# Performance work log

Measured on AMD Instinct MI355X. Metric: run time of the kernel, lower is better.

## Reference

```python
import jax, jax.numpy as jnp
import numpy as np

B, N, F, NCG, NCONV, VOCAB = 16, 1024, 128, 64, 3, 100
EPS = 0.001


def setup_inputs() -> dict:
    key = jax.random.key(0)
    ks = jax.random.split(key, 16)
    atoms_nodes = jax.random.randint(ks[0], (B, N), 0, VOCAB, dtype=jnp.int32)
    xyz = jax.random.normal(ks[1], (B, N, 3), jnp.float32) * 3.0
    # chain bonds (i, i+1) per molecule -> every atom has degree >= 1
    bi = jnp.repeat(jnp.arange(B), N - 1)
    si = jnp.tile(jnp.arange(N - 1), B)
    bonds = jnp.stack([bi, si, si + 1], axis=1).astype(jnp.int32)  # [B*(N-1), 3]
    tau = jnp.float32(1.0)
    gumbel_u = jax.random.uniform(ks[2], (B, N, NCG), jnp.float32, 1e-6, 1.0 - 1e-6)
    # parameters
    emb = jax.random.normal(ks[3], (VOCAB, F), jnp.float32) * 0.1
    emb = emb.at[0].set(0.0)  # padding_idx=0
    s = 1.0 / np.sqrt(F)
    upd_W1 = jax.random.uniform(ks[4], (NCONV, F, F), jnp.float32, -s, s)
    upd_b1 = jax.random.uniform(ks[5], (NCONV, F), jnp.float32, -s, s)
    upd_W2 = jax.random.uniform(ks[6], (NCONV, F, F), jnp.float32, -s, s)
    upd_b2 = jax.random.uniform(ks[7], (NCONV, F), jnp.float32, -s, s)
    cg_W1 = jax.random.uniform(ks[8], (F, F), jnp.float32, -s, s)
    cg_b1 = jax.random.uniform(ks[9], (F,), jnp.float32, -s, s)
    cg_W2 = jax.random.uniform(ks[10], (F, NCG), jnp.float32, -s, s)
    cg_b2 = jax.random.uniform(ks[11], (NCG,), jnp.float32, -s, s)
    return {"atoms_nodes": atoms_nodes, "xyz": xyz, "bonds": bonds, "tau": tau,
            "gumbel_u": gumbel_u, "emb": emb,
            "upd_W1": upd_W1, "upd_b1": upd_b1, "upd_W2": upd_W2, "upd_b2": upd_b2,
            "cg_W1": cg_W1, "cg_b1": cg_b1, "cg_W2": cg_W2, "cg_b2": cg_b2}


def reference(atoms_nodes, xyz, bonds, tau, gumbel_u, emb,
              upd_W1, upd_b1, upd_W2, upd_b2, cg_W1, cg_b1, cg_W2, cg_b2):
    h = emb[atoms_nodes]  # [B,N,F]
    # dense symmetric adjacency from bond list
    adj = jnp.zeros((B, N, N), jnp.float32)
    adj = adj.at[bonds[:, 0], bonds[:, 1], bonds[:, 2]].set(1.0)
    adj = adj.at[bonds[:, 0], bonds[:, 2], bonds[:, 1]].set(1.0)
    deg = jnp.sum(adj, axis=-1)[:, :, None]  # [B,N,1]
    for l in range(NCONV):
        ch = jnp.tanh(h @ upd_W1[l] + upd_b1[l]) @ upd_W2[l] + upd_b2[l]
        dh = jnp.einsum('bif,bij->bjf', ch, adj) / deg
        h = h + dh
    # gumbel-softmax assignment (soft)
    assign_logits = jnp.tanh(h @ cg_W1 + cg_b1) @ cg_W2 + cg_b2  # [B,N,NCG]
    g = -jnp.log(-jnp.log(gumbel_u))
    M = jax.nn.softmax((assign_logits + g) / tau, axis=-1)  # [B,N,NCG]
    M_norm = M / jnp.sum(M, axis=-2, keepdims=True)
    H = jnp.einsum('bnj,bnf->bjf', M_norm, h)        # [B,NCG,F]
    cg_xyz = jnp.einsum('bin,bij->bjn', xyz, M_norm)  # [B,NCG,3]
    cg_adj = jnp.broadcast_to(jnp.ones((NCG, NCG)) - jnp.eye(NCG), (B, NCG, NCG))
    diff = cg_xyz[:, :, None, :] - cg_xyz[:, None, :, :]
    dist = jnp.sqrt(jnp.sum(diff * diff, axis=-1) + EPS)  # [B,NCG,NCG]
    knbrs = jnp.argsort(dist, axis=-1)
    return (M, M_norm, h, H, adj, cg_xyz, cg_adj, knbrs)
```

## Files before the change

### kernel.cpp

```cpp
#include <hip/hip_runtime.h>
#include <math.h>

#define BB 16
#define NN 1024
#define FF 128
#define NCG 64
#define NCONV 3
#define CAP 8

typedef double f64x4 __attribute__((ext_vector_type(4)));

static const size_t O_M     = 0;
static const size_t O_MN    = (size_t)BB*NN*NCG;
static const size_t O_H     = O_MN  + (size_t)BB*NN*NCG;
static const size_t O_HH    = O_H   + (size_t)BB*NN*FF;
static const size_t O_ADJ   = O_HH  + (size_t)BB*NCG*FF;
static const size_t O_CGXYZ = O_ADJ + (size_t)BB*NN*NN;
static const size_t O_CGADJ = O_CGXYZ + (size_t)BB*NCG*3;
static const size_t O_KN    = O_CGADJ + (size_t)BB*NCG*NCG;

static const size_t S_H64   = 0;
static const size_t S_T64   = 2097152;
static const size_t S_C64   = 4194304;
static const size_t S_LM64  = 0;
static const size_t S_COLSP = 4194304;
static const size_t S_HPF   = 6291456;
static const size_t S_CGP   = 7340032;
static const size_t S_NBR   = 7438336;
static const size_t S_W64   = 7503872;

static const size_t WO_CGW1 = 98304;
static const size_t WO_CGW2 = 114688;
static const int    W64_N   = 122880;

static const size_t W_INVD = 0;
static const size_t W_COLS = (size_t)BB*NN;
static const size_t W_CG64 = W_COLS + (size_t)BB*NCG;
static const size_t W_CNT  = W_CG64 + (size_t)BB*NCG*3;

__global__ void k_zero(int* cnt) {
    int i = blockIdx.x * blockDim.x + threadIdx.x;
    if (i < BB*NN) cnt[i] = 0;
}

__global__ void k_build_nbr(const int* __restrict__ bonds, int nb, int* cnt, int* nbr) {
    int i = blockIdx.x * blockDim.x + threadIdx.x;
    if (i >= nb) return;
    int b = bonds[i*3+0], s = bonds[i*3+1], t = bonds[i*3+2];
    int ns = b*NN + s, nt = b*NN + t;
    int p = atomicAdd(&cnt[ns], 1);
    if (p < CAP) nbr[(size_t)ns*CAP + p] = nt;
    int q = atomicAdd(&cnt[nt], 1);
    if (q < CAP) nbr[(size_t)nt*CAP + q] = ns;
}

__global__ void k_invdeg(const int* __restrict__ cnt, double* invdeg) {
    int i = blockIdx.x * blockDim.x + threadIdx.x;
    if (i >= BB*NN) return;
    int d = cnt[i];
    invdeg[i] = d > 0 ? 1.0 / (double)d : 0.0;
}

__global__ void k_cgadj(float* cgadj) {
    int idx = blockIdx.x * blockDim.x + threadIdx.x;
    if (idx >= BB*NCG*NCG) return;
    int i = (idx / NCG) % NCG, j = idx % NCG;
    cgadj[idx] = (i == j) ? 0.f : 1.f;
}

__global__ void k_emb64(const int* __restrict__ atoms, const float* __restrict__ emb,
                        double* __restrict__ h) {
    int idx = blockIdx.x * blockDim.x + threadIdx.x;
    if (idx >= BB*NN*(FF/4)) return;
    int n = idx / (FF/4), f4 = idx % (FF/4);
    int a = atoms[n];
    const float4 v = *reinterpret_cast<const float4*>(&emb[(size_t)a*FF + f4*4]);
    double* hp = &h[(size_t)n*FF + f4*4];
    hp[0] = (double)v.x; hp[1] = (double)v.y; hp[2] = (double)v.z; hp[3] = (double)v.w;
}

__global__ void k_cvtW(const float* __restrict__ uW1, const float* __restrict__ uW2,
                       const float* __restrict__ cgW1, const float* __restrict__ cgW2,
                       double* __restrict__ W64) {
    int idx = blockIdx.x * blockDim.x + threadIdx.x;
    if (idx >= W64_N) return;
    float v;
    if (idx < 98304) {
        int l = idx >> 15, r = idx & 32767;
        v = (r < 16384) ? uW1[l*16384 + r] : uW2[l*16384 + (r & 16383)];
    } else if (idx < 114688) {
        v = cgW1[idx - 98304];
    } else {
        v = cgW2[idx - 114688];
    }
    W64[idx] = (double)v;
}

template<int COUTT, bool TANH>
__global__ __launch_bounds__(256) void k_gemm_mfma(const double* __restrict__ in,
                                                   const double* __restrict__ W,
                                                   const float* __restrict__ bias,
                                                   double* __restrict__ out) {
    constexpr int K = 128, KC = 32;
    constexpr int CT2 = COUTT/2;
    __shared__ double As[64*34];
    __shared__ double Ws[KC*66];
    const int tid = threadIdx.x;
    const int col0 = blockIdx.y * 64;
    const int C02 = col0 >> 1;
    const size_t row0 = (size_t)blockIdx.x * 64;
    const double2* in2 = reinterpret_cast<const double2*>(in + row0*K);
    const double2* Wg2 = reinterpret_cast<const double2*>(W);
    double2* As2 = reinterpret_cast<double2*>(As);
    double2* Ws2 = reinterpret_cast<double2*>(Ws);

    double2 pA[4], pW[4];
    #pragma unroll
    for (int i = 0; i < 4; ++i) { int q = tid + i*256; pA[i] = in2[(q>>4)*64 + (q&15)]; }
    #pragma unroll
    for (int i = 0; i < 4; ++i) { int q = tid + i*256; pW[i] = Wg2[(q>>5)*CT2 + C02 + (q&31)]; }

    const int lane = tid & 63;
    const int wv = tid >> 6;
    const int m = lane & 15, kq = lane >> 4;
    const int arow = (wv*16 + m)*34 + kq;

    f64x4 acc[4];
    #pragma unroll
    for (int ct = 0; ct < 4; ++ct) acc[ct] = (f64x4){0.0, 0.0, 0.0, 0.0};

    for (int kc = 0; kc < K; kc += KC) {
        __syncthreads();
        #pragma unroll
        for (int i = 0; i < 4; ++i) { int q = tid + i*256; As2[(q>>4)*17 + (q&15)] = pA[i]; }
        #pragma unroll
        for (int i = 0; i < 4; ++i) { int q = tid + i*256; Ws2[(q>>5)*33 + (q&31)] = pW[i]; }
        if (kc + KC < K) {
            const int kn = kc + KC, kn2 = kn >> 1;
            #pragma unroll
            for (int i = 0; i < 4; ++i) { int q = tid + i*256; pA[i] = in2[(q>>4)*64 + kn2 + (q&15)]; }
            #pragma unroll
            for (int i = 0; i < 4; ++i) { int q = tid + i*256; pW[i] = Wg2[(kn + (q>>5))*CT2 + C02 + (q&31)]; }
        }
        __syncthreads();
        #pragma unroll
        for (int kk = 0; kk < KC; kk += 4) {
            double a = As[arow + kk];
            const double* wrow = Ws + (kk + kq)*66 + m;
            #pragma unroll
            for (int ct = 0; ct < 4; ++ct) {
                double b = wrow[ct*16];
                acc[ct] = __builtin_amdgcn_mfma_f64_16x16x4f64(a, b, acc[ct], 0, 0, 0);
            }
        }
    }

    const int orow = wv*16 + kq*4;
    #pragma unroll
    for (int ct = 0; ct < 4; ++ct) {
        int c = col0 + ct*16 + m;
        double bv = (double)bias[c];
        #pragma unroll
        for (int i = 0; i < 4; ++i) {
            double v = acc[ct][i] + bv;
            if (TANH) v = tanh(v);
            out[(row0 + orow + i)*COUTT + c] = v;
        }
    }
}

template<bool WRITE_F32>
__global__ void k_gather(const double* __restrict__ ch, const double* __restrict__ invdeg,
                         const int* __restrict__ nbr, const int* __restrict__ cnt,
                         double* __restrict__ h, float* __restrict__ hout) {
    int idx = blockIdx.x * blockDim.x + threadIdx.x;
    if (idx >= BB*NN*(FF/4)) return;
    int node = idx >> 5, f4 = idx & 31;
    int c = cnt[node];
    double2 s0; s0.x = 0.0; s0.y = 0.0;
    double2 s1 = s0;
    for (int q = 0; q < c; ++q) {
        int nb = nbr[(size_t)node*CAP + q];
        const double2* cp = reinterpret_cast<const double2*>(ch + (size_t)nb*FF + f4*4);
        double2 a = cp[0], b2 = cp[1];
        s0.x += a.x; s0.y += a.y; s1.x += b2.x; s1.y += b2.y;
    }
    double w = invdeg[node];
    double2* hp = reinterpret_cast<double2*>(h + (size_t)node*FF + f4*4);
    double2 h0 = hp[0], h1 = hp[1];
    h0.x += s0.x*w; h0.y += s0.y*w; h1.x += s1.x*w; h1.y += s1.y*w;
    hp[0] = h0; hp[1] = h1;
    if (WRITE_F32) {
        float4 o; o.x = (float)h0.x; o.y = (float)h0.y; o.z = (float)h1.x; o.w = (float)h1.y;
        *reinterpret_cast<float4*>(&hout[(size_t)node*FF + f4*4]) = o;
    }
}

__global__ void k_softmax64(double* __restrict__ lm, const float* __restrict__ gum,
                            const float* __restrict__ tau_p, float* __restrict__ M_out) {
    int row = blockIdx.x * 4 + threadIdx.x / 64;
    int lane = threadIdx.x & 63;
    double tau = (double)(*tau_p);
    double u = (double)gum[(size_t)row*NCG + lane];
    double g = -log(-log(u));
    double v = (lm[(size_t)row*NCG + lane] + g) / tau;
    double m = v;
    #pragma unroll
    for (int off = 32; off; off >>= 1) m = fmax(m, __shfl_xor(m, off));
    double e = exp(v - m);
    double s = e;
    #pragma unroll
    for (int off = 32; off; off >>= 1) s += __shfl_xor(s, off);
    double mv = e / s;
    lm[(size_t)row*NCG + lane] = mv;
    M_out[(size_t)row*NCG + lane] = (float)mv;
}

__global__ __launch_bounds__(256) void k_cols_part(const double* __restrict__ M,
                                                   double* __restrict__ colsp) {
    __shared__ double red[256];
    const int b = blockIdx.x, c = blockIdx.y;
    const int tid = threadIdx.x;
    const int j = tid & 63, q = tid >> 6;
    const double* Mb = M + (size_t)b*NN*NCG + (size_t)(c*64 + q*16)*NCG;
    double s = 0.0;
    #pragma unroll
    for (int r = 0; r < 16; ++r) s += Mb[(size_t)r*NCG + j];
    red[tid] = s;
    __syncthreads();
    if (tid < 64)
        colsp[((size_t)b*16 + c)*NCG + j] = red[j] + red[64+j] + red[128+j] + red[192+j];
}

__global__ void k_cols_fin(const double* __restrict__ colsp, double* __restrict__ colsum) {
    int idx = blockIdx.x * blockDim.x + threadIdx.x;
    if (idx >= BB*NCG) return;
    int b = idx >> 6, j = idx & 63;
    double s = 0.0;
    #pragma unroll
    for (int c = 0; c < 16; ++c) s += colsp[((size_t)b*16 + c)*NCG + j];
    colsum[idx] = s;
}

__global__ void k_mnorm_out(const double* __restrict__ M, const double* __restrict__ colsum,
                            float* __restrict__ Mn) {
    size_t i = (size_t)blockIdx.x * blockDim.x + threadIdx.x;
    if (i >= (size_t)BB*NN*NCG) return;
    size_t b = i >> 16;
    int j = (int)(i & 63);
    Mn[i] = (float)(M[i] / colsum[b*NCG + j]);
}

__global__ __launch_bounds__(256) void k_Hpart32(const float* __restrict__ Mn,
                                                 const float* __restrict__ h,
                                                 float* __restrict__ Hp) {
    __shared__ float Ms[32*NCG];
    __shared__ float hs[32*FF];
    const int b = blockIdx.x, ch = blockIdx.y;
    const int tid = threadIdx.x;
    const int tc = tid % 32, tr = tid / 32;
    const float4* M4 = reinterpret_cast<const float4*>(Mn + (size_t)b*NN*NCG);
    const float4* h4 = reinterpret_cast<const float4*>(h + (size_t)b*NN*FF);
    float4* Ms4 = reinterpret_cast<float4*>(Ms);
    float4* hs4 = reinterpret_cast<float4*>(hs);
    const float2* Ms2 = reinterpret_cast<const float2*>(Ms);
    const float2* hs2 = reinterpret_cast<const float2*>(hs);

    float acc[8][4];
    #pragma unroll
    for (int i = 0; i < 8; ++i)
        #pragma unroll
        for (int j = 0; j < 4; ++j) acc[i][j] = 0.f;

    for (int s = 0; s < 2; ++s) {
        const int n0 = ch*64 + s*32;
        __syncthreads();
        #pragma unroll
        for (int i = 0; i < 2; ++i) Ms4[tid + i*256] = M4[n0*16 + tid + i*256];
        #pragma unroll
        for (int i = 0; i < 4; ++i) hs4[tid + i*256] = h4[n0*32 + tid + i*256];
        __syncthreads();
        for (int n = 0; n < 32; ++n) {
            float2 hv0 = hs2[n*64 + tc];
            float2 hv1 = hs2[n*64 + 32 + tc];
            float2 m0 = Ms2[n*32 + tr];
            float2 m1 = Ms2[n*32 + 8 + tr];
            float2 m2 = Ms2[n*32 + 16 + tr];
            float2 m3 = Ms2[n*32 + 24 + tr];
            float mj[8] = {m0.x, m0.y, m1.x, m1.y, m2.x, m2.y, m3.x, m3.y};
            #pragma unroll
            for (int jj = 0; jj < 8; ++jj) {
                acc[jj][0] += mj[jj]*hv0.x; acc[jj][1] += mj[jj]*hv0.y;
                acc[jj][2] += mj[jj]*hv1.x; acc[jj][3] += mj[jj]*hv1.y;
            }
        }
    }
    float* Ho = Hp + ((size_t)ch*BB + b) * NCG * FF;
    #pragma unroll
    for (int gj = 0; gj < 4; ++gj)
        #pragma unroll
        for (int pj = 0; pj < 2; ++pj) {
            int j = tr*2 + gj*16 + pj;
            int jj = gj*2 + pj;
            float2 o0; o0.x = acc[jj][0]; o0.y = acc[jj][1];
            float2 o1; o1.x = acc[jj][2]; o1.y = acc[jj][3];
            float2* op = reinterpret_cast<float2*>(Ho + (size_t)j*FF);
            op[tc] = o0; op[32 + tc] = o1;
        }
}

__global__ void k_Hfin32(const float* __restrict__ Hp, float* __restrict__ H) {
    int idx = blockIdx.x * blockDim.x + threadIdx.x;
    if (idx >= BB*NCG*FF) return;
    int b = idx / (NCG*FF);
    int r = idx % (NCG*FF);
    float s = 0.f;
    #pragma unroll
    for (int c = 0; c < 16; ++c) s += Hp[((size_t)c*BB + b)*NCG*FF + r];
    H[idx] = s;
}

__global__ __launch_bounds__(192) void k_cgpart(const double* __restrict__ M,
                                                const float* __restrict__ xyz,
                                                double* __restrict__ cgp) {
    __shared__ double Ms[32*NCG];
    __shared__ double xs[32*3];
    const int b = blockIdx.x, ch = blockIdx.y;
    const int tid = threadIdx.x;
    const int j = tid / 3, d = tid % 3;
    const int n0 = ch*32;
    const double2* M2 = reinterpret_cast<const double2*>(M + (size_t)b*NN*NCG);
    double2* Ms2 = reinterpret_cast<double2*>(Ms);
    const float* xb = xyz + (size_t)b*NN*3;
    for (int q = tid; q < 1024; q += 192) Ms2[q] = M2[n0*32 + q];
    for (int q = tid; q < 96; q += 192) xs[q] = (double)xb[n0*3 + q];
    __syncthreads();
    double acc = 0.0;
    #pragma unroll 8
    for (int n = 0; n < 32; ++n) acc += Ms[n*NCG + j] * xs[n*3 + d];
    cgp[((size_t)ch*BB + b)*192 + tid] = acc;
}

__global__ void k_cgfin(const double* __restrict__ cgp, const double* __restrict__ colsum,
                        double* __restrict__ cg64, float* __restrict__ cg) {
    int idx = blockIdx.x * blockDim.x + threadIdx.x;
    if (idx >= BB*NCG*3) return;
    int b = idx / (NCG*3);
    int r = idx % (NCG*3);
    int j = r / 3;
    double s = 0.0;
    #pragma unroll
    for (int c = 0; c < 32; ++c) s += cgp[((size_t)c*BB + b)*192 + r];
    double v = s / colsum[b*NCG + j];
    cg64[idx] = v;
    cg[idx] = (float)v;
}

__global__ __launch_bounds__(1024) void k_knbrs(const double* __restrict__ cg,
                                                float* __restrict__ kn) {
    __shared__ double cs[NCG*3];
    const int b = blockIdx.x;
    const int tid = threadIdx.x;
    const int i = blockIdx.y * 16 + tid / 64;
    const int j = tid & 63;
    if (tid < NCG*3) cs[tid] = cg[(size_t)b*NCG*3 + tid];
    __syncthreads();
    double xi = cs[i*3+0], yi = cs[i*3+1], zi = cs[i*3+2];
    double dxj = xi - cs[j*3+0], dyj = yi - cs[j*3+1], dzj = zi - cs[j*3+2];
    double d2j = dxj*dxj + dyj*dyj + dzj*dzj;
    int rank = 0;
    for (int k = 0; k < NCG; ++k) {
        double dx = xi - cs[k*3+0], dy = yi - cs[k*3+1], dz = zi - cs[k*3+2];
        double d2k = dx*dx + dy*dy + dz*dz;
        rank += (d2k < d2j) || (d2k == d2j && k < j);
    }
    kn[(size_t)b*NCG*NCG + (size_t)i*NCG + rank] = (float)j;
}

__global__ void k_zero_adj(float4* adj4, long n4) {
    long i = (long)blockIdx.x * blockDim.x + threadIdx.x;
    long stride = (long)gridDim.x * blockDim.x;
    float4 z; z.x = z.y = z.z = z.w = 0.f;
    for (; i < n4; i += stride) adj4[i] = z;
}

__global__ void k_bonds_adj(const int* __restrict__ bonds, int nb, float* adj) {
    int i = blockIdx.x * blockDim.x + threadIdx.x;
    if (i >= nb) return;
    int b = bonds[i*3+0], s = bonds[i*3+1], t = bonds[i*3+2];
    size_t base = (size_t)b * NN * NN;
    adj[base + (size_t)s*NN + t] = 1.f;
    adj[base + (size_t)t*NN + s] = 1.f;
}

extern "C" void kernel_launch(void* const* d_in, const int* in_sizes, int n_in,
                              void* d_out, int out_size, void* d_ws, size_t ws_size,
                              hipStream_t stream) {
    const int*   atoms  = (const int*)  d_in[0];
    const float* xyz    = (const float*)d_in[1];
    const int*   bonds  = (const int*)  d_in[2];
    const float* tau    = (const float*)d_in[3];
    const float* gum    = (const float*)d_in[4];
    const float* emb    = (const float*)d_in[5];
    const float* uW1    = (const float*)d_in[6];
    const float* ub1    = (const float*)d_in[7];
    const float* uW2    = (const float*)d_in[8];
    const float* ub2    = (const float*)d_in[9];
    const float* cgW1   = (const float*)d_in[10];
    const float* cgb1   = (const float*)d_in[11];
    const float* cgW2   = (const float*)d_in[12];
    const float* cgb2   = (const float*)d_in[13];

    float* out = (float*)d_out;
    float* o_M   = out + O_M;
    float* o_Mn  = out + O_MN;
    float* o_h   = out + O_H;
    float* o_H   = out + O_HH;
    float* o_adj = out + O_ADJ;
    float* o_cg  = out + O_CGXYZ;
    float* o_ca  = out + O_CGADJ;
    float* o_kn  = out + O_KN;

    double* scr   = (double*)o_adj;
    double* h64   = scr + S_H64;
    double* t64   = scr + S_T64;
    double* c64   = scr + S_C64;
    double* lm64  = scr + S_LM64;
    double* colsp = scr + S_COLSP;
    float*  Hpf   = (float*)(scr + S_HPF);
    double* cgp   = scr + S_CGP;
    int*    nbr   = (int*)(scr + S_NBR);
    double* W64   = scr + S_W64;

    double* wsd    = (double*)d_ws;
    double* invdeg = wsd + W_INVD;
    double* colsum = wsd + W_COLS;
    double* cg64   = wsd + W_CG64;
    int*    cnt    = (int*)(wsd + W_CNT);

    const int nb = in_sizes[2] / 3;

    hipLaunchKernelGGL(k_zero, dim3(64), dim3(256), 0, stream, cnt);
    hipLaunchKernelGGL(k_build_nbr, dim3((nb+255)/256), dim3(256), 0, stream,
                       bonds, nb, cnt, nbr);
    hipLaunchKernelGGL(k_invdeg, dim3(64), dim3(256), 0, stream, cnt, invdeg);
    hipLaunchKernelGGL(k_cgadj, dim3(256), dim3(256), 0, stream, o_ca);
    hipLaunchKernelGGL(k_cvtW, dim3((W64_N+255)/256), dim3(256), 0, stream,
                       uW1, uW2, cgW1, cgW2, W64);
    hipLaunchKernelGGL(k_emb64, dim3(2048), dim3(256), 0, stream, atoms, emb, h64);

    for (int l = 0; l < NCONV; ++l) {
        hipLaunchKernelGGL((k_gemm_mfma<128,true>), dim3(256,2), dim3(256), 0, stream,
                           h64, W64 + (size_t)l*32768, ub1 + (size_t)l*FF, t64);
        hipLaunchKernelGGL((k_gemm_mfma<128,false>), dim3(256,2), dim3(256), 0, stream,
                           t64, W64 + (size_t)l*32768 + 16384, ub2 + (size_t)l*FF, c64);
        if (l < NCONV-1)
            hipLaunchKernelGGL((k_gather<false>), dim3(2048), dim3(256), 0, stream,
                               c64, invdeg, nbr, cnt, h64, o_h);
        else
            hipLaunchKernelGGL((k_gather<true>), dim3(2048), dim3(256), 0, stream,
                               c64, invdeg, nbr, cnt, h64, o_h);
    }

    hipLaunchKernelGGL((k_gemm_mfma<128,true>), dim3(256,2), dim3(256), 0, stream,
                       h64, W64 + WO_CGW1, cgb1, t64);
    hipLaunchKernelGGL((k_gemm_mfma<64,false>), dim3(256,1), dim3(256), 0, stream,
                       t64, W64 + WO_CGW2, cgb2, lm64);

    hipLaunchKernelGGL(k_softmax64, dim3(4096), dim3(256), 0, stream,
                       lm64, gum, tau, o_M);
    hipLaunchKernelGGL(k_cols_part, dim3(16,16), dim3(256), 0, stream, lm64, colsp);
    hipLaunchKernelGGL(k_cols_fin, dim3(4), dim3(256), 0, stream, colsp, colsum);
    hipLaunchKernelGGL(k_mnorm_out, dim3(4096), dim3(256), 0, stream, lm64, colsum, o_Mn);
    hipLaunchKernelGGL(k_Hpart32, dim3(BB, 16), dim3(256), 0, stream, o_Mn, o_h, Hpf);
    hipLaunchKernelGGL(k_Hfin32, dim3(512), dim3(256), 0, stream, Hpf, o_H);
    hipLaunchKernelGGL(k_cgpart, dim3(BB, 32), dim3(192), 0, stream, lm64, xyz, cgp);
    hipLaunchKernelGGL(k_cgfin, dim3(12), dim3(256), 0, stream, cgp, colsum, cg64, o_cg);
    hipLaunchKernelGGL(k_knbrs, dim3(BB, 4), dim3(1024), 0, stream, cg64, o_kn);

    hipLaunchKernelGGL(k_zero_adj, dim3(4096), dim3(256), 0, stream,
                       (float4*)o_adj, (long)BB*NN*NN/4);
    hipLaunchKernelGGL(k_bonds_adj, dim3((nb+255)/256), dim3(256), 0, stream,
                       bonds, nb, o_adj);
}
```

Baseline: 369.8 us.

## Fuse neighbor gather into next GEMM, merge init kernels, atomic column sums

Folds the neighbor aggregation and h update of each conv layer into the A-tile load of the following tanh GEMM. That GEMM is either the next layer's first linear or the cg_W1 projection. This removes a separate gather pass and one re-read of h. The small setup kernels (zeroing, weight conversion, cg_adj fill, embedding) are merged into one launch, and invdeg is computed inline. Column sums of M are accumulated with double atomics inside the softmax kernel instead of a two-stage reduction. The trade-offs are a smaller 32-row GEMM tile, irregular gathers inside the GEMM prologue, and atomic contention on 1024 addresses.

```diff
diff --git a/kernel.cpp b/kernel.cpp
--- a/kernel.cpp
+++ b/kernel.cpp
@@ -23,7 +23,6 @@
 static const size_t S_T64   = 2097152;
 static const size_t S_C64   = 4194304;
 static const size_t S_LM64  = 0;
-static const size_t S_COLSP = 4194304;
 static const size_t S_HPF   = 6291456;
 static const size_t S_CGP   = 7340032;
 static const size_t S_NBR   = 7438336;
@@ -33,14 +32,39 @@
 static const size_t WO_CGW2 = 114688;
 static const int    W64_N   = 122880;
 
-static const size_t W_INVD = 0;
-static const size_t W_COLS = (size_t)BB*NN;
-static const size_t W_CG64 = W_COLS + (size_t)BB*NCG;
+static const size_t W_COLS = 0;
+static const size_t W_CG64 = (size_t)BB*NCG;
 static const size_t W_CNT  = W_CG64 + (size_t)BB*NCG*3;
 
-__global__ void k_zero(int* cnt) {
+__global__ void k_init(const int* __restrict__ atoms, const float* __restrict__ emb,
+                       const float* __restrict__ uW1, const float* __restrict__ uW2,
+                       const float* __restrict__ cgW1, const float* __restrict__ cgW2,
+                       double* __restrict__ W64, float* __restrict__ cgadj,
+                       int* __restrict__ cnt, double* __restrict__ colsum,
+                       double* __restrict__ h64) {
     int i = blockIdx.x * blockDim.x + threadIdx.x;
     if (i < BB*NN) cnt[i] = 0;
+    if (i < BB*NCG) colsum[i] = 0.0;
+    if (i < W64_N) {
+        float v;
+        if (i < 98304) {
+            int l = i >> 15, r = i & 32767;
+            v = (r < 16384) ? uW1[l*16384 + r] : uW2[l*16384 + (r & 16383)];
+        } else if (i < 114688) v = cgW1[i - 98304];
+        else                   v = cgW2[i - 114688];
+        W64[i] = (double)v;
+    }
+    if (i < BB*NCG*NCG) {
+        int r = (i / NCG) % NCG, cjj = i % NCG;
+        cgadj[i] = (r == cjj) ? 0.f : 1.f;
+    }
+    if (i < BB*NN*(FF/4)) {
+        int n = i / (FF/4), f4 = i % (FF/4);
+        int a = atoms[n];
+        const float4 v = *reinterpret_cast<const float4*>(&emb[(size_t)a*FF + f4*4]);
+        double* hp = &h64[(size_t)n*FF + f4*4];
+        hp[0] = (double)v.x; hp[1] = (double)v.y; hp[2] = (double)v.z; hp[3] = (double)v.w;
+    }
 }
 
 __global__ void k_build_nbr(const int* __restrict__ bonds, int nb, int* cnt, int* nbr) {
@@ -52,48 +76,6 @@
     if (p < CAP) nbr[(size_t)ns*CAP + p] = nt;
     int q = atomicAdd(&cnt[nt], 1);
     if (q < CAP) nbr[(size_t)nt*CAP + q] = ns;
-}
-
-__global__ void k_invdeg(const int* __restrict__ cnt, double* invdeg) {
-    int i = blockIdx.x * blockDim.x + threadIdx.x;
-    if (i >= BB*NN) return;
-    int d = cnt[i];
-    invdeg[i] = d > 0 ? 1.0 / (double)d : 0.0;
-}
-
-__global__ void k_cgadj(float* cgadj) {
-    int idx = blockIdx.x * blockDim.x + threadIdx.x;
-    if (idx >= BB*NCG*NCG) return;
-    int i = (idx / NCG) % NCG, j = idx % NCG;
-    cgadj[idx] = (i == j) ? 0.f : 1.f;
-}
-
-__global__ void k_emb64(const int* __restrict__ atoms, const float* __restrict__ emb,
-                        double* __restrict__ h) {
-    int idx = blockIdx.x * blockDim.x + threadIdx.x;
-    if (idx >= BB*NN*(FF/4)) return;
-    int n = idx / (FF/4), f4 = idx % (FF/4);
-    int a = atoms[n];
-    const float4 v = *reinterpret_cast<const float4*>(&emb[(size_t)a*FF + f4*4]);
-    double* hp = &h[(size_t)n*FF + f4*4];
-    hp[0] = (double)v.x; hp[1] = (double)v.y; hp[2] = (double)v.z; hp[3] = (double)v.w;
-}
-
-__global__ void k_cvtW(const float* __restrict__ uW1, const float* __restrict__ uW2,
-                       const float* __restrict__ cgW1, const float* __restrict__ cgW2,
-                       double* __restrict__ W64) {
-    int idx = blockIdx.x * blockDim.x + threadIdx.x;
-    if (idx >= W64_N) return;
-    float v;
-    if (idx < 98304) {
-        int l = idx >> 15, r = idx & 32767;
-        v = (r < 16384) ? uW1[l*16384 + r] : uW2[l*16384 + (r & 16383)];
-    } else if (idx < 114688) {
-        v = cgW1[idx - 98304];
-    } else {
-        v = cgW2[idx - 114688];
-    }
-    W64[idx] = (double)v;
 }
 
 template<int COUTT, bool TANH>
@@ -169,35 +151,108 @@
     }
 }
 
-template<bool WRITE_F32>
-__global__ void k_gather(const double* __restrict__ ch, const double* __restrict__ invdeg,
-                         const int* __restrict__ nbr, const int* __restrict__ cnt,
-                         double* __restrict__ h, float* __restrict__ hout) {
-    int idx = blockIdx.x * blockDim.x + threadIdx.x;
-    if (idx >= BB*NN*(FF/4)) return;
-    int node = idx >> 5, f4 = idx & 31;
-    int c = cnt[node];
-    double2 s0; s0.x = 0.0; s0.y = 0.0;
-    double2 s1 = s0;
-    for (int q = 0; q < c; ++q) {
-        int nb = nbr[(size_t)node*CAP + q];
-        const double2* cp = reinterpret_cast<const double2*>(ch + (size_t)nb*FF + f4*4);
-        double2 a = cp[0], b2 = cp[1];
-        s0.x += a.x; s0.y += a.y; s1.x += b2.x; s1.y += b2.y;
-    }
-    double w = invdeg[node];
-    double2* hp = reinterpret_cast<double2*>(h + (size_t)node*FF + f4*4);
-    double2 h0 = hp[0], h1 = hp[1];
-    h0.x += s0.x*w; h0.y += s0.y*w; h1.x += s1.x*w; h1.y += s1.y*w;
-    hp[0] = h0; hp[1] = h1;
-    if (WRITE_F32) {
-        float4 o; o.x = (float)h0.x; o.y = (float)h0.y; o.z = (float)h1.x; o.w = (float)h1.y;
-        *reinterpret_cast<float4*>(&hout[(size_t)node*FF + f4*4]) = o;
+template<bool GATHER, bool WRITE_F32>
+__global__ __launch_bounds__(256) void k_gemm_fg(const double* __restrict__ in,
+        const double* __restrict__ ch, const int* __restrict__ nbr,
+        const int* __restrict__ cnt, const double* __restrict__ W,
+        const float* __restrict__ bias, double* __restrict__ hupd,
+        float* __restrict__ hf32, double* __restrict__ out) {
+    constexpr int K = 128, KC = 32, AST = 130, WST = 130;
+    __shared__ double As[32*AST];
+    __shared__ double Ws[KC*WST];
+    const int tid = threadIdx.x;
+    const size_t row0 = (size_t)blockIdx.x * 32;
+    const double2* Wg2 = reinterpret_cast<const double2*>(W);
+
+    double2 pW[8];
+    #pragma unroll
+    for (int i = 0; i < 8; ++i) { int q = tid + i*256; pW[i] = Wg2[q]; }
+
+    {
+        const int srow = tid >> 3, skg = tid & 7;
+        const size_t grow = row0 + srow;
+        double2 v[8];
+        const double2* hp = reinterpret_cast<const double2*>(in + grow*K) + skg*8;
+        #pragma unroll
+        for (int i = 0; i < 8; ++i) v[i] = hp[i];
+        if (GATHER) {
+            int c = cnt[grow];
+            double w = c > 0 ? 1.0/(double)c : 0.0;
+            for (int q = 0; q < c; ++q) {
+                int nb2 = nbr[grow*CAP + q];
+                const double2* cp = reinterpret_cast<const double2*>(ch + (size_t)nb2*K) + skg*8;
+                #pragma unroll
+                for (int i = 0; i < 8; ++i) { double2 t = cp[i]; v[i].x += w*t.x; v[i].y += w*t.y; }
+            }
+            double2* hg = reinterpret_cast<double2*>(hupd + grow*K) + skg*8;
+            #pragma unroll
+            for (int i = 0; i < 8; ++i) hg[i] = v[i];
+        }
+        if (WRITE_F32) {
+            float4* fp = reinterpret_cast<float4*>(hf32 + grow*K) + skg*4;
+            #pragma unroll
+            for (int i = 0; i < 4; ++i) {
+                float4 o;
+                o.x = (float)v[2*i].x;   o.y = (float)v[2*i].y;
+                o.z = (float)v[2*i+1].x; o.w = (float)v[2*i+1].y;
+                fp[i] = o;
+            }
+        }
+        double2* ap = reinterpret_cast<double2*>(As + srow*AST) + skg*8;
+        #pragma unroll
+        for (int i = 0; i < 8; ++i) ap[i] = v[i];
+    }
+
+    const int lane = tid & 63, wv = tid >> 6;
+    const int wr = wv & 1, wc = wv >> 1;
+    const int m = lane & 15, kq = lane >> 4;
+    const int abase = (wr*16 + m)*AST;
+
+    f64x4 acc[4];
+    #pragma unroll
+    for (int ct = 0; ct < 4; ++ct) acc[ct] = (f64x4){0.0, 0.0, 0.0, 0.0};
+
+    for (int kc = 0; kc < K; kc += KC) {
+        __syncthreads();
+        #pragma unroll
+        for (int i = 0; i < 8; ++i) {
+            int q = tid + i*256;
+            reinterpret_cast<double2*>(Ws + (q>>6)*WST)[q & 63] = pW[i];
+        }
+        if (kc + KC < K) {
+            #pragma unroll
+            for (int i = 0; i < 8; ++i) {
+                int q = tid + i*256;
+                pW[i] = Wg2[(kc + KC + (q>>6))*64 + (q & 63)];
+            }
+        }
+        __syncthreads();
+        #pragma unroll
+        for (int kk = 0; kk < KC; kk += 4) {
+            double a = As[abase + kc + kk + kq];
+            const double* wrow = Ws + (kk + kq)*WST + wc*64 + m;
+            #pragma unroll
+            for (int ct = 0; ct < 4; ++ct) {
+                double b = wrow[ct*16];
+                acc[ct] = __builtin_amdgcn_mfma_f64_16x16x4f64(a, b, acc[ct], 0, 0, 0);
+            }
+        }
+    }
+
+    const int orow = wr*16 + kq*4;
+    #pragma unroll
+    for (int ct = 0; ct < 4; ++ct) {
+        int c = wc*64 + ct*16 + m;
+        double bv = (double)bias[c];
+        #pragma unroll
+        for (int i = 0; i < 4; ++i)
+            out[(row0 + orow + i)*K + c] = tanh(acc[ct][i] + bv);
     }
 }
 
 __global__ void k_softmax64(double* __restrict__ lm, const float* __restrict__ gum,
-                            const float* __restrict__ tau_p, float* __restrict__ M_out) {
+                            const float* __restrict__ tau_p, float* __restrict__ M_out,
+                            double* __restrict__ colsum) {
     int row = blockIdx.x * 4 + threadIdx.x / 64;
     int lane = threadIdx.x & 63;
     double tau = (double)(*tau_p);
@@ -214,32 +269,7 @@
     double mv = e / s;
     lm[(size_t)row*NCG + lane] = mv;
     M_out[(size_t)row*NCG + lane] = (float)mv;
-}
-
-__global__ __launch_bounds__(256) void k_cols_part(const double* __restrict__ M,
-                                                   double* __restrict__ colsp) {
-    __shared__ double red[256];
-    const int b = blockIdx.x, c = blockIdx.y;
-    const int tid = threadIdx.x;
-    const int j = tid & 63, q = tid >> 6;
-    const double* Mb = M + (size_t)b*NN*NCG + (size_t)(c*64 + q*16)*NCG;
-    double s = 0.0;
-    #pragma unroll
-    for (int r = 0; r < 16; ++r) s += Mb[(size_t)r*NCG + j];
-    red[tid] = s;
-    __syncthreads();
-    if (tid < 64)
-        colsp[((size_t)b*16 + c)*NCG + j] = red[j] + red[64+j] + red[128+j] + red[192+j];
-}
-
-__global__ void k_cols_fin(const double* __restrict__ colsp, double* __restrict__ colsum) {
-    int idx = blockIdx.x * blockDim.x + threadIdx.x;
-    if (idx >= BB*NCG) return;
-    int b = idx >> 6, j = idx & 63;
-    double s = 0.0;
-    #pragma unroll
-    for (int c = 0; c < 16; ++c) s += colsp[((size_t)b*16 + c)*NCG + j];
-    colsum[idx] = s;
+    atomicAdd(&colsum[(row >> 10) * NCG + lane], mv);
 }
 
 __global__ void k_mnorm_out(const double* __restrict__ M, const double* __restrict__ colsum,
@@ -426,51 +456,42 @@
     double* t64   = scr + S_T64;
     double* c64   = scr + S_C64;
     double* lm64  = scr + S_LM64;
-    double* colsp = scr + S_COLSP;
     float*  Hpf   = (float*)(scr + S_HPF);
     double* cgp   = scr + S_CGP;
     int*    nbr   = (int*)(scr + S_NBR);
     double* W64   = scr + S_W64;
 
     double* wsd    = (double*)d_ws;
-    double* invdeg = wsd + W_INVD;
     double* colsum = wsd + W_COLS;
     double* cg64   = wsd + W_CG64;
     int*    cnt    = (int*)(wsd + W_CNT);
 
     const int nb = in_sizes[2] / 3;
 
-    hipLaunchKernelGGL(k_zero, dim3(64), dim3(256), 0, stream, cnt);
+    hipLaunchKernelGGL(k_init, dim3(2048), dim3(256), 0, stream,
+                       atoms, emb, uW1, uW2, cgW1, cgW2, W64, o_ca, cnt, colsum, h64);
     hipLaunchKernelGGL(k_build_nbr, dim3((nb+255)/256), dim3(256), 0, stream,
                        bonds, nb, cnt, nbr);
-    hipLaunchKernelGGL(k_invdeg, dim3(64), dim3(256), 0, stream, cnt, invdeg);
-    hipLaunchKernelGGL(k_cgadj, dim3(256), dim3(256), 0, stream, o_ca);
-    hipLaunchKernelGGL(k_cvtW, dim3((W64_N+255)/256), dim3(256), 0, stream,
-                       uW1, uW2, cgW1, cgW2, W64);
-    hipLaunchKernelGGL(k_emb64, dim3(2048), dim3(256), 0, stream, atoms, emb, h64);
-
-    for (int l = 0; l < NCONV; ++l) {
-        hipLaunchKernelGGL((k_gemm_mfma<128,true>), dim3(256,2), dim3(256), 0, stream,
-                           h64, W64 + (size_t)l*32768, ub1 + (size_t)l*FF, t64);
-        hipLaunchKernelGGL((k_gemm_mfma<128,false>), dim3(256,2), dim3(256), 0, stream,
-                           t64, W64 + (size_t)l*32768 + 16384, ub2 + (size_t)l*FF, c64);
-        if (l < NCONV-1)
-            hipLaunchKernelGGL((k_gather<false>), dim3(2048), dim3(256), 0, stream,
-                               c64, invdeg, nbr, cnt, h64, o_h);
-        else
-            hipLaunchKernelGGL((k_gather<true>), dim3(2048), dim3(256), 0, stream,
-                               c64, invdeg, nbr, cnt, h64, o_h);
-    }
 
     hipLaunchKernelGGL((k_gemm_mfma<128,true>), dim3(256,2), dim3(256), 0, stream,
-                       h64, W64 + WO_CGW1, cgb1, t64);
+                       h64, W64, ub1, t64);
+    hipLaunchKernelGGL((k_gemm_mfma<128,false>), dim3(256,2), dim3(256), 0, stream,
+                       t64, W64 + 16384, ub2, c64);
+    hipLaunchKernelGGL((k_gemm_fg<true,false>), dim3(512), dim3(256), 0, stream,
+                       h64, c64, nbr, cnt, W64 + 32768, ub1 + FF, h64, o_h, t64);
+    hipLaunchKernelGGL((k_gemm_mfma<128,false>), dim3(256,2), dim3(256), 0, stream,
+                       t64, W64 + 32768 + 16384, ub2 + FF, c64);
+    hipLaunchKernelGGL((k_gemm_fg<true,false>), dim3(512), dim3(256), 0, stream,
+                       h64, c64, nbr, cnt, W64 + 65536, ub1 + 2*FF, h64, o_h, t64);
+    hipLaunchKernelGGL((k_gemm_mfma<128,false>), dim3(256,2), dim3(256), 0, stream,
+                       t64, W64 + 65536 + 16384, ub2 + 2*FF, c64);
+    hipLaunchKernelGGL((k_gemm_fg<true,true>), dim3(512), dim3(256), 0, stream,
+                       h64, c64, nbr, cnt, W64 + WO_CGW1, cgb1, h64, o_h, t64);
     hipLaunchKernelGGL((k_gemm_mfma<64,false>), dim3(256,1), dim3(256), 0, stream,
                        t64, W64 + WO_CGW2, cgb2, lm64);
 
     hipLaunchKernelGGL(k_softmax64, dim3(4096), dim3(256), 0, stream,
-                       lm64, gum, tau, o_M);
-    hipLaunchKernelGGL(k_cols_part, dim3(16,16), dim3(256), 0, stream, lm64, colsp);
-    hipLaunchKernelGGL(k_cols_fin, dim3(4), dim3(256), 0, stream, colsp, colsum);
+                       lm64, gum, tau, o_M, colsum);
     hipLaunchKernelGGL(k_mnorm_out, dim3(4096), dim3(256), 0, stream, lm64, colsum, o_Mn);
     hipLaunchKernelGGL(k_Hpart32, dim3(BB, 16), dim3(256), 0, stream, o_Mn, o_h, Hpf);
     hipLaunchKernelGGL(k_Hfin32, dim3(512), dim3(256), 0, stream, Hpf, o_H);
```

After: 380.8 us. 1.03x slower.

## Fuse init kernels, fold column sums into softmax, build adjacency from neighbor lists

Applied to the files above, without the earlier changes.

Merges the zero, weight conversion, cg_adj fill and embedding kernels into one init launch. The inverse degree is now computed inside the gather, and column sums are accumulated with atomics inside the softmax kernel. The cg_xyz finalize is folded into the knbrs kernel. The separate zero-fill plus bond scatter of the dense adjacency becomes one per-row kernel that writes zeros and ones from the neighbor list. This cuts launch count and one full pass over the 64 MB adjacency, at the cost of nondeterministic atomic summation order and a CAP-limited neighbor list defining the adjacency.

```diff
diff --git a/kernel.cpp b/kernel.cpp
--- a/kernel.cpp
+++ b/kernel.cpp
@@ -23,24 +23,47 @@
 static const size_t S_T64   = 2097152;
 static const size_t S_C64   = 4194304;
 static const size_t S_LM64  = 0;
-static const size_t S_COLSP = 4194304;
 static const size_t S_HPF   = 6291456;
 static const size_t S_CGP   = 7340032;
-static const size_t S_NBR   = 7438336;
 static const size_t S_W64   = 7503872;
 
 static const size_t WO_CGW1 = 98304;
 static const size_t WO_CGW2 = 114688;
 static const int    W64_N   = 122880;
 
-static const size_t W_INVD = 0;
-static const size_t W_COLS = (size_t)BB*NN;
-static const size_t W_CG64 = W_COLS + (size_t)BB*NCG;
-static const size_t W_CNT  = W_CG64 + (size_t)BB*NCG*3;
-
-__global__ void k_zero(int* cnt) {
+static const size_t W_COLS = 0;
+static const size_t W_CNT  = (size_t)BB*NCG;
+static const size_t W_NBR  = W_CNT + (size_t)BB*NN/2;
+
+__global__ void k_init(const int* __restrict__ atoms, const float* __restrict__ emb,
+                       const float* __restrict__ uW1, const float* __restrict__ uW2,
+                       const float* __restrict__ cgW1, const float* __restrict__ cgW2,
+                       double* __restrict__ W64, float* __restrict__ cgadj,
+                       int* __restrict__ cnt, double* __restrict__ colsum,
+                       double* __restrict__ h64) {
     int i = blockIdx.x * blockDim.x + threadIdx.x;
     if (i < BB*NN) cnt[i] = 0;
+    if (i < BB*NCG) colsum[i] = 0.0;
+    if (i < W64_N) {
+        float v;
+        if (i < 98304) {
+            int l = i >> 15, r = i & 32767;
+            v = (r < 16384) ? uW1[l*16384 + r] : uW2[l*16384 + (r & 16383)];
+        } else if (i < 114688) v = cgW1[i - 98304];
+        else                   v = cgW2[i - 114688];
+        W64[i] = (double)v;
+    }
+    if (i < BB*NCG*NCG) {
+        int r = (i / NCG) % NCG, cjj = i % NCG;
+        cgadj[i] = (r == cjj) ? 0.f : 1.f;
+    }
+    if (i < BB*NN*(FF/4)) {
+        int n = i / (FF/4), f4 = i % (FF/4);
+        int a = atoms[n];
+        const float4 v = *reinterpret_cast<const float4*>(&emb[(size_t)a*FF + f4*4]);
+        double* hp = &h64[(size_t)n*FF + f4*4];
+        hp[0] = (double)v.x; hp[1] = (double)v.y; hp[2] = (double)v.z; hp[3] = (double)v.w;
+    }
 }
 
 __global__ void k_build_nbr(const int* __restrict__ bonds, int nb, int* cnt, int* nbr) {
@@ -52,48 +75,6 @@
     if (p < CAP) nbr[(size_t)ns*CAP + p] = nt;
     int q = atomicAdd(&cnt[nt], 1);
     if (q < CAP) nbr[(size_t)nt*CAP + q] = ns;
-}
-
-__global__ void k_invdeg(const int* __restrict__ cnt, double* invdeg) {
-    int i = blockIdx.x * blockDim.x + threadIdx.x;
-    if (i >= BB*NN) return;
-    int d = cnt[i];
-    invdeg[i] = d > 0 ? 1.0 / (double)d : 0.0;
-}
-
-__global__ void k_cgadj(float* cgadj) {
-    int idx = blockIdx.x * blockDim.x + threadIdx.x;
-    if (idx >= BB*NCG*NCG) return;
-    int i = (idx / NCG) % NCG, j = idx % NCG;
-    cgadj[idx] = (i == j) ? 0.f : 1.f;
-}
-
-__global__ void k_emb64(const int* __restrict__ atoms, const float* __restrict__ emb,
-                        double* __restrict__ h) {
-    int idx = blockIdx.x * blockDim.x + threadIdx.x;
-    if (idx >= BB*NN*(FF/4)) return;
-    int n = idx / (FF/4), f4 = idx % (FF/4);
-    int a = atoms[n];
-    const float4 v = *reinterpret_cast<const float4*>(&emb[(size_t)a*FF + f4*4]);
-    double* hp = &h[(size_t)n*FF + f4*4];
-    hp[0] = (double)v.x; hp[1] = (double)v.y; hp[2] = (double)v.z; hp[3] = (double)v.w;
-}
-
-__global__ void k_cvtW(const float* __restrict__ uW1, const float* __restrict__ uW2,
-                       const float* __restrict__ cgW1, const float* __restrict__ cgW2,
-                       double* __restrict__ W64) {
-    int idx = blockIdx.x * blockDim.x + threadIdx.x;
-    if (idx >= W64_N) return;
-    float v;
-    if (idx < 98304) {
-        int l = idx >> 15, r = idx & 32767;
-        v = (r < 16384) ? uW1[l*16384 + r] : uW2[l*16384 + (r & 16383)];
-    } else if (idx < 114688) {
-        v = cgW1[idx - 98304];
-    } else {
-        v = cgW2[idx - 114688];
-    }
-    W64[idx] = (double)v;
 }
 
 template<int COUTT, bool TANH>
@@ -170,9 +151,9 @@
 }
 
 template<bool WRITE_F32>
-__global__ void k_gather(const double* __restrict__ ch, const double* __restrict__ invdeg,
-                         const int* __restrict__ nbr, const int* __restrict__ cnt,
-                         double* __restrict__ h, float* __restrict__ hout) {
+__global__ void k_gather(const double* __restrict__ ch, const int* __restrict__ nbr,
+                         const int* __restrict__ cnt, double* __restrict__ h,
+                         float* __restrict__ hout) {
     int idx = blockIdx.x * blockDim.x + threadIdx.x;
     if (idx >= BB*NN*(FF/4)) return;
     int node = idx >> 5, f4 = idx & 31;
@@ -185,7 +166,7 @@
         double2 a = cp[0], b2 = cp[1];
         s0.x += a.x; s0.y += a.y; s1.x += b2.x; s1.y += b2.y;
     }
-    double w = invdeg[node];
+    double w = c > 0 ? 1.0/(double)c : 0.0;
     double2* hp = reinterpret_cast<double2*>(h + (size_t)node*FF + f4*4);
     double2 h0 = hp[0], h1 = hp[1];
     h0.x += s0.x*w; h0.y += s0.y*w; h1.x += s1.x*w; h1.y += s1.y*w;
@@ -196,8 +177,11 @@
     }
 }
 
-__global__ void k_softmax64(double* __restrict__ lm, const float* __restrict__ gum,
-                            const float* __restrict__ tau_p, float* __restrict__ M_out) {
+__global__ __launch_bounds__(256) void k_softmax64(double* __restrict__ lm,
+                            const float* __restrict__ gum,
+                            const float* __restrict__ tau_p, float* __restrict__ M_out,
+                            double* __restrict__ colsum) {
+    __shared__ double red[256];
     int row = blockIdx.x * 4 + threadIdx.x / 64;
     int lane = threadIdx.x & 63;
     double tau = (double)(*tau_p);
@@ -214,32 +198,13 @@
     double mv = e / s;
     lm[(size_t)row*NCG + lane] = mv;
     M_out[(size_t)row*NCG + lane] = (float)mv;
-}
-
-__global__ __launch_bounds__(256) void k_cols_part(const double* __restrict__ M,
-                                                   double* __restrict__ colsp) {
-    __shared__ double red[256];
-    const int b = blockIdx.x, c = blockIdx.y;
-    const int tid = threadIdx.x;
-    const int j = tid & 63, q = tid >> 6;
-    const double* Mb = M + (size_t)b*NN*NCG + (size_t)(c*64 + q*16)*NCG;
-    double s = 0.0;
-    #pragma unroll
-    for (int r = 0; r < 16; ++r) s += Mb[(size_t)r*NCG + j];
-    red[tid] = s;
+    red[threadIdx.x] = mv;
     __syncthreads();
-    if (tid < 64)
-        colsp[((size_t)b*16 + c)*NCG + j] = red[j] + red[64+j] + red[128+j] + red[192+j];
-}
-
-__global__ void k_cols_fin(const double* __restrict__ colsp, double* __restrict__ colsum) {
-    int idx = blockIdx.x * blockDim.x + threadIdx.x;
-    if (idx >= BB*NCG) return;
-    int b = idx >> 6, j = idx & 63;
-    double s = 0.0;
-    #pragma unroll
-    for (int c = 0; c < 16; ++c) s += colsp[((size_t)b*16 + c)*NCG + j];
-    colsum[idx] = s;
+    if (threadIdx.x < 64) {
+        int b = row >> 10;
+        atomicAdd(&colsum[b*NCG + lane],
+                  red[lane] + red[64+lane] + red[128+lane] + red[192+lane]);
+    }
 }
 
 __global__ void k_mnorm_out(const double* __restrict__ M, const double* __restrict__ colsum,
@@ -341,30 +306,24 @@
     cgp[((size_t)ch*BB + b)*192 + tid] = acc;
 }
 
-__global__ void k_cgfin(const double* __restrict__ cgp, const double* __restrict__ colsum,
-                        double* __restrict__ cg64, float* __restrict__ cg) {
-    int idx = blockIdx.x * blockDim.x + threadIdx.x;
-    if (idx >= BB*NCG*3) return;
-    int b = idx / (NCG*3);
-    int r = idx % (NCG*3);
-    int j = r / 3;
-    double s = 0.0;
-    #pragma unroll
-    for (int c = 0; c < 32; ++c) s += cgp[((size_t)c*BB + b)*192 + r];
-    double v = s / colsum[b*NCG + j];
-    cg64[idx] = v;
-    cg[idx] = (float)v;
-}
-
-__global__ __launch_bounds__(1024) void k_knbrs(const double* __restrict__ cg,
+__global__ __launch_bounds__(1024) void k_knbrs(const double* __restrict__ cgp,
+                                                const double* __restrict__ colsum,
+                                                float* __restrict__ o_cg,
                                                 float* __restrict__ kn) {
     __shared__ double cs[NCG*3];
     const int b = blockIdx.x;
     const int tid = threadIdx.x;
+    if (tid < NCG*3) {
+        double s = 0.0;
+        #pragma unroll
+        for (int c = 0; c < 32; ++c) s += cgp[((size_t)c*BB + b)*192 + tid];
+        double v = s / colsum[b*NCG + tid/3];
+        cs[tid] = v;
+        if (blockIdx.y == 0) o_cg[(size_t)b*192 + tid] = (float)v;
+    }
+    __syncthreads();
     const int i = blockIdx.y * 16 + tid / 64;
     const int j = tid & 63;
-    if (tid < NCG*3) cs[tid] = cg[(size_t)b*NCG*3 + tid];
-    __syncthreads();
     double xi = cs[i*3+0], yi = cs[i*3+1], zi = cs[i*3+2];
     double dxj = xi - cs[j*3+0], dyj = yi - cs[j*3+1], dzj = zi - cs[j*3+2];
     double d2j = dxj*dxj + dyj*dyj + dzj*dzj;
@@ -377,20 +336,24 @@
     kn[(size_t)b*NCG*NCG + (size_t)i*NCG + rank] = (float)j;
 }
 
-__global__ void k_zero_adj(float4* adj4, long n4) {
-    long i = (long)blockIdx.x * blockDim.x + threadIdx.x;
-    long stride = (long)gridDim.x * blockDim.x;
-    float4 z; z.x = z.y = z.z = z.w = 0.f;
-    for (; i < n4; i += stride) adj4[i] = z;
-}
-
-__global__ void k_bonds_adj(const int* __restrict__ bonds, int nb, float* adj) {
-    int i = blockIdx.x * blockDim.x + threadIdx.x;
-    if (i >= nb) return;
-    int b = bonds[i*3+0], s = bonds[i*3+1], t = bonds[i*3+2];
-    size_t base = (size_t)b * NN * NN;
-    adj[base + (size_t)s*NN + t] = 1.f;
-    adj[base + (size_t)t*NN + s] = 1.f;
+__global__ __launch_bounds__(256) void k_adj(const int* __restrict__ cnt,
+                                             const int* __restrict__ nbr,
+                                             float4* __restrict__ adj4) {
+    const int node = blockIdx.x;
+    const int t = threadIdx.x;
+    const int col0 = t*4;
+    int c = cnt[node];
+    if (c > CAP) c = CAP;
+    float4 v; v.x = v.y = v.z = v.w = 0.f;
+    for (int q = 0; q < c; ++q) {
+        int dst = nbr[(size_t)node*CAP + q] & (NN-1);
+        int d = dst - col0;
+        if (d == 0) v.x = 1.f;
+        else if (d == 1) v.y = 1.f;
+        else if (d == 2) v.z = 1.f;
+        else if (d == 3) v.w = 1.f;
+    }
+    adj4[(size_t)node*256 + t] = v;
 }
 
 extern "C" void kernel_launch(void* const* d_in, const int* in_sizes, int n_in,
@@ -426,28 +389,21 @@
     double* t64   = scr + S_T64;
     double* c64   = scr + S_C64;
     double* lm64  = scr + S_LM64;
-    double* colsp = scr + S_COLSP;
     float*  Hpf   = (float*)(scr + S_HPF);
     double* cgp   = scr + S_CGP;
-    int*    nbr   = (int*)(scr + S_NBR);
     double* W64   = scr + S_W64;
 
     double* wsd    = (double*)d_ws;
-    double* invdeg = wsd + W_INVD;
     double* colsum = wsd + W_COLS;
-    double* cg64   = wsd + W_CG64;
     int*    cnt    = (int*)(wsd + W_CNT);
+    int*    nbr    = (int*)(wsd + W_NBR);
 
     const int nb = in_sizes[2] / 3;
 
-    hipLaunchKernelGGL(k_zero, dim3(64), dim3(256), 0, stream, cnt);
+    hipLaunchKernelGGL(k_init, dim3(2048), dim3(256), 0, stream,
+                       atoms, emb, uW1, uW2, cgW1, cgW2, W64, o_ca, cnt, colsum, h64);
     hipLaunchKernelGGL(k_build_nbr, dim3((nb+255)/256), dim3(256), 0, stream,
                        bonds, nb, cnt, nbr);
-    hipLaunchKernelGGL(k_invdeg, dim3(64), dim3(256), 0, stream, cnt, invdeg);
-    hipLaunchKernelGGL(k_cgadj, dim3(256), dim3(256), 0, stream, o_ca);
-    hipLaunchKernelGGL(k_cvtW, dim3((W64_N+255)/256), dim3(256), 0, stream,
-                       uW1, uW2, cgW1, cgW2, W64);
-    hipLaunchKernelGGL(k_emb64, dim3(2048), dim3(256), 0, stream, atoms, emb, h64);
 
     for (int l = 0; l < NCONV; ++l) {
         hipLaunchKernelGGL((k_gemm_mfma<128,true>), dim3(256,2), dim3(256), 0, stream,
@@ -456,10 +412,10 @@
                            t64, W64 + (size_t)l*32768 + 16384, ub2 + (size_t)l*FF, c64);
         if (l < NCONV-1)
             hipLaunchKernelGGL((k_gather<false>), dim3(2048), dim3(256), 0, stream,
-                               c64, invdeg, nbr, cnt, h64, o_h);
+                               c64, nbr, cnt, h64, o_h);
         else
             hipLaunchKernelGGL((k_gather<true>), dim3(2048), dim3(256), 0, stream,
-                               c64, invdeg, nbr, cnt, h64, o_h);
+                               c64, nbr, cnt, h64, o_h);
     }
 
     hipLaunchKernelGGL((k_gemm_mfma<128,true>), dim3(256,2), dim3(256), 0, stream,
@@ -468,18 +424,14 @@
                        t64, W64 + WO_CGW2, cgb2, lm64);
 
     hipLaunchKernelGGL(k_softmax64, dim3(4096), dim3(256), 0, stream,
-                       lm64, gum, tau, o_M);
-    hipLaunchKernelGGL(k_cols_part, dim3(16,16), dim3(256), 0, stream, lm64, colsp);
-    hipLaunchKernelGGL(k_cols_fin, dim3(4), dim3(256), 0, stream, colsp, colsum);
+                       lm64, gum, tau, o_M, colsum);
     hipLaunchKernelGGL(k_mnorm_out, dim3(4096), dim3(256), 0, stream, lm64, colsum, o_Mn);
     hipLaunchKernelGGL(k_Hpart32, dim3(BB, 16), dim3(256), 0, stream, o_Mn, o_h, Hpf);
     hipLaunchKernelGGL(k_Hfin32, dim3(512), dim3(256), 0, stream, Hpf, o_H);
     hipLaunchKernelGGL(k_cgpart, dim3(BB, 32), dim3(192), 0, stream, lm64, xyz, cgp);
-    hipLaunchKernelGGL(k_cgfin, dim3(12), dim3(256), 0, stream, cgp, colsum, cg64, o_cg);
-    hipLaunchKernelGGL(k_knbrs, dim3(BB, 4), dim3(1024), 0, stream, cg64, o_kn);
-
-    hipLaunchKernelGGL(k_zero_adj, dim3(4096), dim3(256), 0, stream,
-                       (float4*)o_adj, (long)BB*NN*NN/4);
-    hipLaunchKernelGGL(k_bonds_adj, dim3((nb+255)/256), dim3(256), 0, stream,
-                       bonds, nb, o_adj);
-}
+    hipLaunchKernelGGL(k_knbrs, dim3(BB, 4), dim3(1024), 0, stream,
+                       cgp, colsum, o_cg, o_kn);
+
+    hipLaunchKernelGGL(k_adj, dim3(BB*NN), dim3(256), 0, stream,
+                       cnt, nbr, (float4*)o_adj);
+}
```

New measurement: 361.2 us. -2.3%, faster.
